# Performance work log

Hardware: AMD Instinct MI355X
Metric: run time of the kernel (lower is better)

Reference implementation:

```python
import jax, jax.numpy as jnp
import numpy as np
from jax import lax

# --- Clifford algebra Cl(3,0): sig_g = [1,1,1], n_blades = 8 ---
SIG = np.array([1.0, 1.0, 1.0], dtype=np.float32)
N_GEN = len(SIG)
N_BLADES = 1 << N_GEN

def _build_cayley(g):
    # Structure constants C[a,b,c]: e_a * e_b = C[a,b,a^b] * e_{a^b}
    n = len(g); nb = 1 << n
    C = np.zeros((nb, nb, nb), dtype=np.float32)
    for a in range(nb):
        for b in range(nb):
            s = 1.0
            x = a >> 1
            while x:
                if bin(x & b).count('1') % 2:
                    s = -s
                x >>= 1
            common = a & b
            for k in range(n):
                if (common >> k) & 1:
                    s *= g[k]
            C[a, b, a ^ b] = s
    return C

CAYLEY = _build_cayley(SIG)
# blade signs: scalar coefficient of e_i * e_i (metric square of each blade)
BLADE_SIGNS = np.array([CAYLEY[i, i, 0] for i in range(N_BLADES)], dtype=np.float32)

DT = 0.1      # EPEngine dt
N_FREE = 5    # EPEngine n_free

def _energy(h, input_mv, W_rec, C, signs):
    # h: [B,L,H,I]
    rho = jnp.clip(h, 0.0, 1.0)
    E_self = 0.5 * jnp.sum(h * h, axis=(1, 2, 3))                       # [B]
    E_in = jnp.einsum('blhi,blhi,i->b', rho, input_mv, signs)           # [B]
    # causal recurrent term: geometric product of h_{l-1} with W_rec
    rec = jnp.einsum('blhi,ghj,ijk->blgk', rho[:, :-1], W_rec, C)       # [B,L-1,H,I]
    E_rec = jnp.einsum('blhk,blhk,k->b', rho[:, 1:], rec, signs)        # [B]
    return E_self - E_in - E_rec

def _free_phase(h0, input_mv, W_rec, C, signs):
    gfn = jax.grad(lambda h: jnp.sum(_energy(h, input_mv, W_rec, C, signs)))
    def step(h, _):
        return h - DT * gfn(h), None
    h, _ = lax.scan(step, h0, None, length=N_FREE)
    return h

def setup_inputs() -> dict:
    key = jax.random.key(0)
    ks = jax.random.split(key, 5)
    B, L, V, E, H = 4, 256, 32000, 256, 256
    x = jax.random.randint(ks[0], (B, L), 0, V)
    emb_table = jax.random.normal(ks[1], (V, E), jnp.float32)
    W_in = jax.random.normal(ks[2], (H, E, N_BLADES), jnp.float32) * 0.1
    W_rec = jax.random.normal(ks[3], (H, H, N_BLADES), jnp.float32) * 0.05
    W_out = jax.random.normal(ks[4], (V, H, N_BLADES), jnp.float32) * 0.1
    return {"x": x, "emb_table": emb_table, "W_in": W_in, "W_rec": W_rec, "W_out": W_out}

def reference(x, emb_table, W_in, W_rec, W_out):
    C = jnp.asarray(CAYLEY)
    signs = jnp.asarray(BLADE_SIGNS)
    emb = emb_table[x]                                  # [B,L,E]
    input_mv = jnp.einsum('bld,hdi->blhi', emb, W_in)   # [B,L,H,I]
    B, L = x.shape
    H = W_in.shape[0]
    h0 = jnp.zeros((B, L, H, N_BLADES), jnp.float32)
    h_free = _free_phase(h0, input_mv, W_rec, C, signs) # [B,L,H,I]
    # scalar part of geometric product of h_free with W_out (only blade 0 kept)
    logits = jnp.einsum('blhi,vhj,ij->blv', h_free, W_out, C[:, :, 0])
    return logits
```

## Files before the change

### kernel.cpp

```cpp
#include <hip/hip_runtime.h>
#include <cstddef>
#include <cstdint>

#define VOCAB  32000
#define EMB    256
#define NB     8
#define KDIM   2048
#define NROWS  1024
#define NCOL   4096
#define LLEN   256

typedef __attribute__((ext_vector_type(8))) short short8;
typedef __attribute__((ext_vector_type(4))) float f32x4;
typedef __attribute__((ext_vector_type(16))) float f32x16;
typedef __attribute__((ext_vector_type(4))) int i32x4;
typedef __attribute__((ext_vector_type(16))) int i32x16;

__device__ __forceinline__ float cl3_sign(int a, int b) {
  int x = a >> 1, p = 0;
  while (x) { p ^= __popc(x & b) & 1; x >>= 1; }
  return p ? -1.f : 1.f;
}

__device__ __forceinline__ float clipf(float v) { return fminf(fmaxf(v, 0.f), 1.f); }

__device__ __forceinline__ unsigned short f2bf(float f) {
  unsigned u = __float_as_uint(f);
  u += 0x7FFF + ((u >> 16) & 1);
  return (unsigned short)(u >> 16);
}
__device__ __forceinline__ float bf2f(unsigned short h) {
  return __uint_as_float(((unsigned)h) << 16);
}

__device__ __forceinline__ void gload16(const void* g, void* l) {
  __builtin_amdgcn_global_load_lds((const __attribute__((address_space(1))) uint32_t*)g,
                                   (__attribute__((address_space(3))) uint32_t*)l, 16, 0, 0);
}

__device__ __forceinline__ float dig_inv(float mx) {
  return exp2f((float)(5 - ilogbf(fmaxf(mx, 1e-20f))));
}

__device__ __forceinline__ size_t bfoff(int rt, int k, int r) {
  return ((size_t)(rt * 128 + (k >> 4)) << 11) + (size_t)(((k >> 3) & 1) << 10) + ((r & 127) << 3) + (k & 7);
}

__global__ __launch_bounds__(256) void k_build_mrt(const float* __restrict__ Wrec,
                                                   unsigned short* __restrict__ Mhi,
                                                   unsigned short* __restrict__ Mlo) {
  const int t = threadIdx.x;
  const int b = blockIdx.x;
  if (b < 2048) {
    const int n = b, h = t;
    const int g = n >> 3, kb = n & 7;
    const float* src = Wrec + (size_t)g * KDIM + h * 8;
    float w[8];
    *(float4*)&w[0] = *(const float4*)src;
    *(float4*)&w[4] = *(const float4*)(src + 4);
    short8 H, L;
#pragma unroll
    for (int i = 0; i < 8; ++i) {
      int j = i ^ kb;
      float v = w[j] * cl3_sign(i, j);
      unsigned short hi = f2bf(v);
      H[i] = (short)hi;
      L[i] = (short)f2bf(v - bf2f(hi));
    }
    size_t off = ((size_t)((n >> 7) * 128 + (h >> 1)) << 11) + ((size_t)(h & 1) << 10) + ((n & 127) << 3);
    *(short8*)&Mhi[off] = H;
    *(short8*)&Mlo[off] = L;
  } else {
    const int h = b - 2048, p = t;
    const float* src = Wrec + (size_t)h * KDIM + p * 8;
    float w[8];
    *(float4*)&w[0] = *(const float4*)src;
    *(float4*)&w[4] = *(const float4*)(src + 4);
    const int slabn = 16 + (p >> 4);
    const size_t baseo = ((size_t)(slabn * 128 + (h >> 1)) << 11) + ((size_t)(h & 1) << 10);
#pragma unroll
    for (int q = 0; q < 8; ++q) {
      int r = (p & 15) * 8 + q;
      short8 H, L;
#pragma unroll
      for (int i = 0; i < 8; ++i) {
        int j = q ^ i;
        float v = cl3_sign(i, i) * cl3_sign(q, j) * w[j];
        unsigned short hi = f2bf(v);
        H[i] = (short)hi;
        L[i] = (short)f2bf(v - bf2f(hi));
      }
      size_t off = baseo + (r << 3);
      *(short8*)&Mhi[off] = H;
      *(short8*)&Mlo[off] = L;
    }
  }
}

__global__ __launch_bounds__(256) void k_dig_wout(const float* __restrict__ W,
                                                  float* __restrict__ sB,
                                                  char* __restrict__ Wd1,
                                                  char* __restrict__ Wd2) {
  __shared__ float ld[4 * 2052];
  __shared__ float rmax[4];
  const int t = threadIdx.x;
  const int bid = blockIdx.x;
  const float* src = W + (size_t)bid * 8192;
#pragma unroll
  for (int i = 0; i < 8; ++i) {
    int f = i * 256 + t;
    int row = f >> 9, c4 = f & 511;
    float4 v = ((const float4*)src)[f];
    *(float4*)&ld[row * 2052 + c4 * 4] = v;
  }
  __syncthreads();
  const int w = t >> 6, l = t & 63;
  float m = 0.f;
#pragma unroll
  for (int j = 0; j < 8; ++j) {
    float4 v = *(const float4*)&ld[w * 2052 + (j * 64 + l) * 4];
    m = fmaxf(m, fmaxf(fmaxf(fabsf(v.x), fabsf(v.y)), fmaxf(fabsf(v.z), fabsf(v.w))));
  }
#pragma unroll
  for (int s = 1; s < 64; s <<= 1) m = fmaxf(m, __shfl_xor(m, s));
  m = fmaxf(m, 1e-20f);
  if (l == 0) { rmax[w] = m; sB[bid * 4 + w] = exp2f((float)(ilogbf(m) + 2)); }
  __syncthreads();
  const int rloc = t & 3;
  const int rowg = bid * 4 + rloc;
  const int rowtile = rowg >> 7, rowin = rowg & 127;
  const float inv = dig_inv(rmax[rloc]);
#pragma unroll
  for (int it = 0; it < 2; ++it) {
    int c16 = (t >> 2) + it * 64;
    char d1[16], d2[16];
#pragma unroll
    for (int j = 0; j < 16; ++j) {
      float tv = ld[rloc * 2052 + c16 * 16 + j] * inv;
      float f1 = rintf(tv);
      d1[j] = (char)(int)f1;
      d2[j] = (char)(int)rintf((tv - f1) * 128.f);
    }
    size_t addr = ((size_t)(rowtile * 64 + (c16 >> 1)) << 12) + (size_t)((c16 & 1) << 11) + (rowin << 4);
    *(i32x4*)&Wd1[addr] = *(i32x4*)d1;
    *(i32x4*)&Wd2[addr] = *(i32x4*)d2;
  }
}

__global__ __launch_bounds__(256) void k_input_h1(const int* __restrict__ x,
                                                  const float* __restrict__ emb,
                                                  const float* __restrict__ Win,
                                                  float* __restrict__ Imv,
                                                  float* __restrict__ Hb,
                                                  unsigned short* __restrict__ Hhi,
                                                  unsigned short* __restrict__ Hlo) {
  __shared__ float se[4][EMB];
  int r0 = blockIdx.x * 4;
  int t = threadIdx.x;
  for (int rr = 0; rr < 4; ++rr) {
    int tok = x[r0 + rr];
    se[rr][t] = emb[(size_t)tok * EMB + t];
  }
  __syncthreads();
  float acc[4][8];
#pragma unroll
  for (int rr = 0; rr < 4; ++rr)
#pragma unroll
    for (int i = 0; i < 8; ++i) acc[rr][i] = 0.f;
  const float* wrow = Win + (size_t)t * KDIM;
  for (int d = 0; d < EMB; ++d) {
    float4 w0 = *(const float4*)(wrow + d * 8);
    float4 w1 = *(const float4*)(wrow + d * 8 + 4);
#pragma unroll
    for (int rr = 0; rr < 4; ++rr) {
      float e = se[rr][d];
      acc[rr][0] += e * w0.x; acc[rr][1] += e * w0.y;
      acc[rr][2] += e * w0.z; acc[rr][3] += e * w0.w;
      acc[rr][4] += e * w1.x; acc[rr][5] += e * w1.y;
      acc[rr][6] += e * w1.z; acc[rr][7] += e * w1.w;
    }
  }
  const int c = t * 8;
  for (int rr = 0; rr < 4; ++rr) {
    int r = r0 + rr;
    float* o = Imv + (size_t)r * KDIM + c;
    *(float4*)o = make_float4(acc[rr][0], acc[rr][1], acc[rr][2], acc[rr][3]);
    *(float4*)(o + 4) = make_float4(acc[rr][4], acc[rr][5], acc[rr][6], acc[rr][7]);
    float hn[8];
    short8 h8, l8;
#pragma unroll
    for (int j = 0; j < 8; ++j) {
      float f = acc[rr][j] * (((0xE8 >> j) & 1) ? -1.f : 1.f);
      hn[j] = 0.f - 0.1f * (0.f - 0.5f * f);
      float a = clipf(hn[j]);
      unsigned short hi = f2bf(a);
      h8[j] = (short)hi;
      l8[j] = (short)f2bf(a - bf2f(hi));
    }
    float* hb = Hb + (size_t)r * KDIM + c;
    *(float4*)hb = make_float4(hn[0], hn[1], hn[2], hn[3]);
    *(float4*)(hb + 4) = make_float4(hn[4], hn[5], hn[6], hn[7]);
    size_t off = bfoff(r >> 7, c, r);
    *(short8*)&Hhi[off] = h8;
    *(short8*)&Hlo[off] = l8;
  }
}

__global__ __launch_bounds__(256, 2) void k_gemm_pre(const unsigned short* __restrict__ Ahi,
                                                     const unsigned short* __restrict__ Alo,
                                                     const unsigned short* __restrict__ Bhi,
                                                     const unsigned short* __restrict__ Blo,
                                                     float* __restrict__ RF0,
                                                     float* __restrict__ RF1) {
  __shared__ __align__(16) char lds[3 * 16384];
  const int b = blockIdx.x;
  const int lin = (b & 7) * 64 + (b >> 3);
  const int half = lin >> 8;
  const int rest = lin & 255;
  const int tm = rest & 7, tn = rest >> 3;
  const int ktbase = half * 64;
  float* __restrict__ C = half ? RF1 : RF0;
  const int t = threadIdx.x;
  const int l = t & 63, w = t >> 6;
  const int wr = w >> 1, wc = w & 1;
  const int wo = w << 10;

  const char* aHg = (const char*)Ahi + (((size_t)(tm * 128 + ktbase)) << 12) + (t << 4);
  const char* aLg = (const char*)Alo + (((size_t)(tm * 128 + ktbase)) << 12) + (t << 4);
  const char* bHg = (const char*)Bhi + (((size_t)(tn * 128 + ktbase)) << 12) + (t << 4);
  const char* bLg = (const char*)Blo + (((size_t)(tn * 128 + ktbase)) << 12) + (t << 4);

  f32x16 acc[2][2];
#pragma unroll
  for (int i = 0; i < 2; ++i)
#pragma unroll
    for (int j = 0; j < 2; ++j) acc[i][j] = (f32x16)0.f;

  auto STAGE = [&](int bf, int kt) {
    char* lb = &lds[bf * 16384];
    size_t kb = (size_t)kt << 12;
    gload16(aHg + kb, lb + wo);
    gload16(aLg + kb, lb + 4096 + wo);
    gload16(bHg + kb, lb + 8192 + wo);
    gload16(bLg + kb, lb + 12288 + wo);
  };

  STAGE(0, 0); STAGE(1, 1);

  const int ra = wr * 64 + (l & 31);
  const int rb = wc * 64 + (l & 31);
  const int cho = (l >> 5) << 11;
  int cur = 0;
  for (int kt = 0; kt < 64; ++kt) {
    int pf = cur + 2; if (pf >= 3) pf -= 3;
    if (kt < 63) { asm volatile("s_waitcnt vmcnt(4)" ::: "memory"); }
    else         { asm volatile("s_waitcnt vmcnt(0)" ::: "memory"); }
    __builtin_amdgcn_s_barrier();
    const char* lb = &lds[cur * 16384];
    short8 ah[2], al[2], bh[2], bl[2];
#pragma unroll
    for (int mi = 0; mi < 2; ++mi) {
      int off = cho + ((ra + mi * 32) << 4);
      ah[mi] = *(const short8*)(lb + off);
      al[mi] = *(const short8*)(lb + 4096 + off);
    }
#pragma unroll
    for (int nj = 0; nj < 2; ++nj) {
      int off = cho + ((rb + nj * 32) << 4);
      bh[nj] = *(const short8*)(lb + 8192 + off);
      bl[nj] = *(const short8*)(lb + 12288 + off);
    }
    if (kt + 2 < 64) STAGE(pf, kt + 2);
    __builtin_amdgcn_s_setprio(1);
#pragma unroll
    for (int mi = 0; mi < 2; ++mi)
#pragma unroll
      for (int nj = 0; nj < 2; ++nj) {
        acc[mi][nj] = __builtin_amdgcn_mfma_f32_32x32x16_bf16(ah[mi], bh[nj], acc[mi][nj], 0, 0, 0);
        acc[mi][nj] = __builtin_amdgcn_mfma_f32_32x32x16_bf16(ah[mi], bl[nj], acc[mi][nj], 0, 0, 0);
        acc[mi][nj] = __builtin_amdgcn_mfma_f32_32x32x16_bf16(al[mi], bh[nj], acc[mi][nj], 0, 0, 0);
      }
    __builtin_amdgcn_s_setprio(0);
    cur = (cur == 2) ? 0 : cur + 1;
  }

  const int rg0 = tm * 128 + wr * 64 + ((l >> 5) << 2);
  const int cg0 = tn * 128 + wc * 64 + (l & 31);
#pragma unroll
  for (int mi = 0; mi < 2; ++mi)
#pragma unroll
    for (int nj = 0; nj < 2; ++nj) {
      f32x16 v = acc[mi][nj];
#pragma unroll
      for (int g = 0; g < 16; ++g) {
        int rr = (g & 3) + ((g >> 2) << 3);
        C[(size_t)(rg0 + mi * 32 + rr) * NCOL + cg0 + nj * 32] = v[g];
      }
    }
}

__global__ __launch_bounds__(256, 2) void k_gemm_i8(const char* __restrict__ Ad1,
                                                    const char* __restrict__ Ad2,
                                                    const char* __restrict__ Bd1,
                                                    const char* __restrict__ Bd2,
                                                    const float* __restrict__ sA,
                                                    const float* __restrict__ sB,
                                                    float* __restrict__ C) {
  __shared__ __align__(16) char lds[3 * 16384];
  const int b = blockIdx.x;
  const int lin = (b & 7) * 250 + (b >> 3);
  const int tm = lin & 7, tn = lin >> 3;
  const int t = threadIdx.x;
  const int l = t & 63, w = t >> 6;
  const int wr = w >> 1, wc = w & 1;
  const int wo = w << 10;

  const char* a1g = Ad1 + (((size_t)tm * 64) << 12) + (t << 4);
  const char* a2g = Ad2 + (((size_t)tm * 64) << 12) + (t << 4);
  const char* b1g = Bd1 + (((size_t)tn * 64) << 12) + (t << 4);
  const char* b2g = Bd2 + (((size_t)tn * 64) << 12) + (t << 4);

  i32x16 acc1[2][2], acc2[2][2];
#pragma unroll
  for (int i = 0; i < 2; ++i)
#pragma unroll
    for (int j = 0; j < 2; ++j) { acc1[i][j] = (i32x16)0; acc2[i][j] = (i32x16)0; }

  auto STAGE = [&](int bf, int kt) {
    char* lb = &lds[bf * 16384];
    size_t kb = (size_t)kt << 12;
    gload16(a1g + kb, lb + wo);
    gload16(a2g + kb, lb + 4096 + wo);
    gload16(b1g + kb, lb + 8192 + wo);
    gload16(b2g + kb, lb + 12288 + wo);
  };

  STAGE(0, 0); STAGE(1, 1);

  const int ra = wr * 64 + (l & 31);
  const int rb = wc * 64 + (l & 31);
  const int kqo = (l >> 5) << 11;
  int cur = 0;
  for (int kt = 0; kt < 64; ++kt) {
    int pf = cur + 2; if (pf >= 3) pf -= 3;
    if (kt < 63) { asm volatile("s_waitcnt vmcnt(4)" ::: "memory"); }
    else         { asm volatile("s_waitcnt vmcnt(0)" ::: "memory"); }
    __builtin_amdgcn_s_barrier();
    const char* lb = &lds[cur * 16384];
    i32x4 a1[2], a2[2], b1[2], b2[2];
#pragma unroll
    for (int mi = 0; mi < 2; ++mi) {
      int off = kqo + ((ra + mi * 32) << 4);
      a1[mi] = *(const i32x4*)(lb + off);
      a2[mi] = *(const i32x4*)(lb + 4096 + off);
    }
#pragma unroll
    for (int nj = 0; nj < 2; ++nj) {
      int off = kqo + ((rb + nj * 32) << 4);
      b1[nj] = *(const i32x4*)(lb + 8192 + off);
      b2[nj] = *(const i32x4*)(lb + 12288 + off);
    }
    if (kt + 2 < 64) STAGE(pf, kt + 2);
    __builtin_amdgcn_s_setprio(1);
#pragma unroll
    for (int mi = 0; mi < 2; ++mi)
#pragma unroll
      for (int nj = 0; nj < 2; ++nj) {
        acc1[mi][nj] = __builtin_amdgcn_mfma_i32_32x32x32_i8(a1[mi], b1[nj], acc1[mi][nj], 0, 0, 0);
        acc2[mi][nj] = __builtin_amdgcn_mfma_i32_32x32x32_i8(a1[mi], b2[nj], acc2[mi][nj], 0, 0, 0);
        acc2[mi][nj] = __builtin_amdgcn_mfma_i32_32x32x32_i8(a2[mi], b1[nj], acc2[mi][nj], 0, 0, 0);
      }
    __builtin_amdgcn_s_setprio(0);
    cur = (cur == 2) ? 0 : cur + 1;
  }

  const int rbase = tm * 128 + wr * 64 + ((l >> 5) << 2);
  const int cb = tn * 128 + wc * 64 + (l & 31);
#pragma unroll
  for (int mi = 0; mi < 2; ++mi)
#pragma unroll
    for (int nj = 0; nj < 2; ++nj) {
      float sBv = sB[cb + nj * 32] * (1.f / 16384.f);
#pragma unroll
      for (int g = 0; g < 16; ++g) {
        int rr = (g & 3) + ((g >> 2) << 3);
        int row = rbase + mi * 32 + rr;
        float c1 = sA[row] * sBv;
        C[(size_t)row * VOCAB + cb + nj * 32] =
            fmaf((float)acc2[mi][nj][g], c1 * (1.f / 128.f), (float)acc1[mi][nj][g] * c1);
      }
    }
}

template <int LAST>
__global__ __launch_bounds__(256) void k_update(float* __restrict__ Hb, const float* __restrict__ Imv,
                                                const float* __restrict__ RF0, const float* __restrict__ RF1,
                                                unsigned short* __restrict__ Hhi,
                                                unsigned short* __restrict__ Hlo,
                                                float* __restrict__ sA,
                                                char* __restrict__ Ad1,
                                                char* __restrict__ Ad2,
                                                int big) {
  __shared__ float red[256];
  int tix = threadIdx.x;
  int idx = blockIdx.x * 256 + tix;
  int r = idx >> 8;
  int c = (idx & 255) << 3;
  int m = r & (LLEN - 1);
  const size_t base = (size_t)r * KDIM + c;
  float h[8], f[8];
  *(float4*)&h[0] = *(const float4*)(Hb + base);
  *(float4*)&h[4] = *(const float4*)(Hb + base + 4);
  float4 i0 = *(const float4*)(Imv + base);
  float4 i1 = *(const float4*)(Imv + base + 4);
  f[0] = i0.x; f[1] = i0.y; f[2] = i0.z; f[3] = i0.w;
  f[4] = i1.x; f[5] = i1.y; f[6] = i1.z; f[7] = i1.w;
#pragma unroll
  for (int j = 0; j < 8; ++j) f[j] *= ((0xE8 >> j) & 1) ? -1.f : 1.f;
  if (m >= 1) {
    const float* rp0 = RF0 + (size_t)(r - 1) * NCOL + c;
    const float* rp1 = RF1 + (size_t)(r - 1) * NCOL + c;
#pragma unroll
    for (int j = 0; j < 8; ++j)
      f[j] += (rp0[j] + rp1[j]) * (((0xE8 >> j) & 1) ? -1.f : 1.f);
  }
  if (m < LLEN - 1) {
    const float* rn0 = RF0 + (size_t)(r + 1) * NCOL + KDIM + c;
    const float* rn1 = RF1 + (size_t)(r + 1) * NCOL + KDIM + c;
#pragma unroll
    for (int j = 0; j < 8; ++j) f[j] += rn0[j] + rn1[j];
  }
  float hn[8], av[8];
#pragma unroll
  for (int j = 0; j < 8; ++j) {
    float hv = h[j];
    float dr = (hv > 0.f && hv < 1.f) ? 1.f : ((hv == 0.f || hv == 1.f) ? 0.5f : 0.f);
    hn[j] = hv - 0.1f * (hv - dr * f[j]);
  }
  *(float4*)(Hb + base) = make_float4(hn[0], hn[1], hn[2], hn[3]);
  *(float4*)(Hb + base + 4) = make_float4(hn[4], hn[5], hn[6], hn[7]);
  if (!LAST) {
    short8 h8, l8;
#pragma unroll
    for (int j = 0; j < 8; ++j) {
      float a = clipf(hn[j]);
      unsigned short hi = f2bf(a);
      h8[j] = (short)hi;
      l8[j] = (short)f2bf(a - bf2f(hi));
    }
    size_t off = bfoff(r >> 7, c, r);
    *(short8*)&Hhi[off] = h8;
    *(short8*)&Hlo[off] = l8;
  } else {
    if (!big) return;
#pragma unroll
    for (int j = 0; j < 8; ++j) av[j] = hn[j] * (((0xE8 >> j) & 1) ? -1.f : 1.f);
    float lm = 0.f;
#pragma unroll
    for (int j = 0; j < 8; ++j) lm = fmaxf(lm, fabsf(av[j]));
    red[tix] = lm; __syncthreads();
    for (int s = 128; s; s >>= 1) { if (tix < s) red[tix] = fmaxf(red[tix], red[tix + s]); __syncthreads(); }
    float mx = fmaxf(red[0], 1e-20f);
    float inv = dig_inv(mx);
    if (tix == 0) sA[r] = exp2f((float)(ilogbf(mx) + 2));
    char d1[8], d2[8];
#pragma unroll
    for (int j = 0; j < 8; ++j) {
      float tv = av[j] * inv;
      float f1 = rintf(tv);
      d1[j] = (char)(int)f1;
      d2[j] = (char)(int)rintf((tv - f1) * 128.f);
    }
    size_t addr = ((size_t)((r >> 7) * 64 + (c >> 5)) << 12) + (size_t)(((c >> 4) & 1) << 11)
                + ((r & 127) << 4) + (c & 15);
    *(uint64_t*)&Ad1[addr] = *(uint64_t*)d1;
    *(uint64_t*)&Ad2[addr] = *(uint64_t*)d2;
  }
}

template <int AMODE>
__global__ __launch_bounds__(256) void k_gemm_split(const float* __restrict__ A,
                                                    const float* __restrict__ B,
                                                    float* __restrict__ C, int ldc) {
  __shared__ unsigned short Ah[128 * 32], Al[128 * 32];
  __shared__ unsigned short Bh[128 * 32], Bl[128 * 32];
  const int t = threadIdx.x;
  const int row0 = blockIdx.y * 128, col0 = blockIdx.x * 128;
  const int l = t & 63, w = t >> 6;
  const int wr = w >> 1, wc = w & 1;
  const int sr = t >> 3;
  const int cc = (t & 7) << 2;
  const int chunkb = cc >> 3;
  const int halfo = (cc >> 2) & 1;
  f32x4 acc[4][4];
#pragma unroll
  for (int i = 0; i < 4; ++i)
#pragma unroll
    for (int j = 0; j < 4; ++j) acc[i][j] = (f32x4)0.f;
  const float sA0 = 1.f;
  const float sA1 = (cc & 4) ? -1.f : 1.f;
  const float sA2 = sA1;
  const float sA3 = -1.f;
  for (int k0 = 0; k0 < KDIM; k0 += 32) {
    float4 va[4], vb[4];
#pragma unroll
    for (int i = 0; i < 4; ++i) {
      va[i] = *(const float4*)(A + (size_t)(row0 + sr + i * 32) * KDIM + k0 + cc);
      vb[i] = *(const float4*)(B + (size_t)(col0 + sr + i * 32) * KDIM + k0 + cc);
    }
    __syncthreads();
#pragma unroll
    for (int i = 0; i < 4; ++i) {
      int row = sr + i * 32;
      int idx = row * 32 + ((chunkb ^ (row & 3)) << 3) + (halfo << 2);
      float4 a = va[i];
      if (AMODE == 0) {
        a.x = clipf(a.x); a.y = clipf(a.y); a.z = clipf(a.z); a.w = clipf(a.w);
      } else {
        a.x *= sA0; a.y *= sA1; a.z *= sA2; a.w *= sA3;
      }
      ushort4 h4, l4;
      h4.x = f2bf(a.x); l4.x = f2bf(a.x - bf2f(h4.x));
      h4.y = f2bf(a.y); l4.y = f2bf(a.y - bf2f(h4.y));
      h4.z = f2bf(a.z); l4.z = f2bf(a.z - bf2f(h4.z));
      h4.w = f2bf(a.w); l4.w = f2bf(a.w - bf2f(h4.w));
      *(ushort4*)&Ah[idx] = h4;
      *(ushort4*)&Al[idx] = l4;
      float4 bb = vb[i];
      h4.x = f2bf(bb.x); l4.x = f2bf(bb.x - bf2f(h4.x));
      h4.y = f2bf(bb.y); l4.y = f2bf(bb.y - bf2f(h4.y));
      h4.z = f2bf(bb.z); l4.z = f2bf(bb.z - bf2f(h4.z));
      h4.w = f2bf(bb.w); l4.w = f2bf(bb.w - bf2f(h4.w));
      *(ushort4*)&Bh[idx] = h4;
      *(ushort4*)&Bl[idx] = l4;
    }
    __syncthreads();
    short8 ah[4], al[4], bh[4], bl[4];
#pragma unroll
    for (int mi = 0; mi < 4; ++mi) {
      int ar = wr * 64 + mi * 16 + (l & 15);
      int kc = (l >> 4) ^ (ar & 3);
      ah[mi] = *(short8*)&Ah[ar * 32 + kc * 8];
      al[mi] = *(short8*)&Al[ar * 32 + kc * 8];
      int br = wc * 64 + mi * 16 + (l & 15);
      int kb = (l >> 4) ^ (br & 3);
      bh[mi] = *(short8*)&Bh[br * 32 + kb * 8];
      bl[mi] = *(short8*)&Bl[br * 32 + kb * 8];
    }
#pragma unroll
    for (int mi = 0; mi < 4; ++mi)
#pragma unroll
      for (int ni = 0; ni < 4; ++ni) {
        acc[mi][ni] = __builtin_amdgcn_mfma_f32_16x16x32_bf16(ah[mi], bh[ni], acc[mi][ni], 0, 0, 0);
        acc[mi][ni] = __builtin_amdgcn_mfma_f32_16x16x32_bf16(ah[mi], bl[ni], acc[mi][ni], 0, 0, 0);
        acc[mi][ni] = __builtin_amdgcn_mfma_f32_16x16x32_bf16(al[mi], bh[ni], acc[mi][ni], 0, 0, 0);
      }
  }
#pragma unroll
  for (int mi = 0; mi < 4; ++mi)
#pragma unroll
    for (int ni = 0; ni < 4; ++ni) {
      int rg = row0 + wr * 64 + mi * 16 + (l >> 4) * 4;
      int cg = col0 + wc * 64 + ni * 16 + (l & 15);
#pragma unroll
      for (int j = 0; j < 4; ++j)
        C[(size_t)(rg + j) * ldc + cg] = acc[mi][ni][j];
    }
}

extern "C" void kernel_launch(void* const* d_in, const int* in_sizes, int n_in,
                              void* d_out, int out_size, void* d_ws, size_t ws_size,
                              hipStream_t stream) {
  const int*   x    = (const int*)d_in[0];
  const float* emb  = (const float*)d_in[1];
  const float* Win  = (const float*)d_in[2];
  const float* Wrec = (const float*)d_in[3];
  const float* Wout = (const float*)d_in[4];
  float* logits = (float*)d_out;

  char* base = (char*)d_ws;
  const size_t MB = 1ull << 20;
  float* Hbuf = (float*)(base + 0);
  float* Imv  = (float*)(base + 8 * MB);
  float* RF0  = (float*)(base + 16 * MB);
  float* RF1  = (float*)(base + 32 * MB);
  unsigned short* Hhi = (unsigned short*)(base + 48 * MB);
  unsigned short* Hlo = (unsigned short*)(base + 52 * MB);
  unsigned short* Mhi = (unsigned short*)(base + 56 * MB);
  unsigned short* Mlo = (unsigned short*)(base + 72 * MB);
  float* sA  = (float*)(base + 88 * MB);
  float* sB  = (float*)(base + 88 * MB + 4096);
  char* Wd1  = base + 88 * MB + 160 * 1024;
  char* Wd2  = Wd1 + (size_t)VOCAB * KDIM;
  char* Ad1  = (char*)Mhi;
  char* Ad2  = (char*)Mlo;

  const size_t need = (size_t)(Wd2 - base) + (size_t)VOCAB * KDIM;
  const bool big = ws_size >= need;

  k_build_mrt<<<2304, 256, 0, stream>>>(Wrec, Mhi, Mlo);
  k_input_h1<<<256, 256, 0, stream>>>(x, emb, Win, Imv, Hbuf, Hhi, Hlo);
  if (big) {
    k_dig_wout<<<8000, 256, 0, stream>>>(Wout, sB, Wd1, Wd2);
  }

  for (int it = 1; it < 5; ++it) {
    k_gemm_pre<<<512, 256, 0, stream>>>(Hhi, Hlo, Mhi, Mlo, RF0, RF1);
    if (it < 4) k_update<0><<<1024, 256, 0, stream>>>(Hbuf, Imv, RF0, RF1, Hhi, Hlo, sA, Ad1, Ad2, big);
    else        k_update<1><<<1024, 256, 0, stream>>>(Hbuf, Imv, RF0, RF1, Hhi, Hlo, sA, Ad1, Ad2, big);
  }

  if (big) {
    k_gemm_i8<<<2000, 256, 0, stream>>>(Ad1, Ad2, Wd1, Wd2, sA, sB, logits);
  } else {
    k_gemm_split<1><<<dim3(VOCAB / 128, NROWS / 128), 256, 0, stream>>>(Hbuf, Wout, logits, VOCAB);
  }
}
```

Baseline: 650.7 us.

## Load GEMM fragments directly from global memory instead of LDS staging

```diff
diff --git a/kernel.cpp b/kernel.cpp
--- a/kernel.cpp
+++ b/kernel.cpp
@@ -31,11 +31,6 @@
 }
 __device__ __forceinline__ float bf2f(unsigned short h) {
   return __uint_as_float(((unsigned)h) << 16);
-}
-
-__device__ __forceinline__ void gload16(const void* g, void* l) {
-  __builtin_amdgcn_global_load_lds((const __attribute__((address_space(1))) uint32_t*)g,
-                                   (__attribute__((address_space(3))) uint32_t*)l, 16, 0, 0);
 }
 
 __device__ __forceinline__ float dig_inv(float mx) {
@@ -212,7 +207,6 @@
                                                      const unsigned short* __restrict__ Blo,
                                                      float* __restrict__ RF0,
                                                      float* __restrict__ RF1) {
-  __shared__ __align__(16) char lds[3 * 16384];
   const int b = blockIdx.x;
   const int lin = (b & 7) * 64 + (b >> 3);
   const int half = lin >> 8;
@@ -223,54 +217,32 @@
   const int t = threadIdx.x;
   const int l = t & 63, w = t >> 6;
   const int wr = w >> 1, wc = w & 1;
-  const int wo = w << 10;
-
-  const char* aHg = (const char*)Ahi + (((size_t)(tm * 128 + ktbase)) << 12) + (t << 4);
-  const char* aLg = (const char*)Alo + (((size_t)(tm * 128 + ktbase)) << 12) + (t << 4);
-  const char* bHg = (const char*)Bhi + (((size_t)(tn * 128 + ktbase)) << 12) + (t << 4);
-  const char* bLg = (const char*)Blo + (((size_t)(tn * 128 + ktbase)) << 12) + (t << 4);
-
-  f32x16 acc[2][2];
-#pragma unroll
-  for (int i = 0; i < 2; ++i)
-#pragma unroll
-    for (int j = 0; j < 2; ++j) acc[i][j] = (f32x16)0.f;
-
-  auto STAGE = [&](int bf, int kt) {
-    char* lb = &lds[bf * 16384];
-    size_t kb = (size_t)kt << 12;
-    gload16(aHg + kb, lb + wo);
-    gload16(aLg + kb, lb + 4096 + wo);
-    gload16(bHg + kb, lb + 8192 + wo);
-    gload16(bLg + kb, lb + 12288 + wo);
-  };
-
-  STAGE(0, 0); STAGE(1, 1);
 
   const int ra = wr * 64 + (l & 31);
   const int rb = wc * 64 + (l & 31);
   const int cho = (l >> 5) << 11;
-  int cur = 0;
+
+  const size_t aOff = (((size_t)(tm * 128 + ktbase)) << 12) + cho + ((size_t)ra << 4);
+  const size_t bOff = (((size_t)(tn * 128 + ktbase)) << 12) + cho + ((size_t)rb << 4);
+  const char* aH = (const char*)Ahi + aOff;
+  const char* aL = (const char*)Alo + aOff;
+  const char* bH = (const char*)Bhi + bOff;
+  const char* bL = (const char*)Blo + bOff;
+
+  f32x16 acc[2][2];
+#pragma unroll
+  for (int i = 0; i < 2; ++i)
+#pragma unroll
+    for (int j = 0; j < 2; ++j) acc[i][j] = (f32x16)0.f;
+
+#pragma unroll 2
   for (int kt = 0; kt < 64; ++kt) {
-    int pf = cur + 2; if (pf >= 3) pf -= 3;
-    if (kt < 63) { asm volatile("s_waitcnt vmcnt(4)" ::: "memory"); }
-    else         { asm volatile("s_waitcnt vmcnt(0)" ::: "memory"); }
-    __builtin_amdgcn_s_barrier();
-    const char* lb = &lds[cur * 16384];
+    size_t o = (size_t)kt << 12;
     short8 ah[2], al[2], bh[2], bl[2];
-#pragma unroll
-    for (int mi = 0; mi < 2; ++mi) {
-      int off = cho + ((ra + mi * 32) << 4);
-      ah[mi] = *(const short8*)(lb + off);
-      al[mi] = *(const short8*)(lb + 4096 + off);
-    }
-#pragma unroll
-    for (int nj = 0; nj < 2; ++nj) {
-      int off = cho + ((rb + nj * 32) << 4);
-      bh[nj] = *(const short8*)(lb + 8192 + off);
-      bl[nj] = *(const short8*)(lb + 12288 + off);
-    }
-    if (kt + 2 < 64) STAGE(pf, kt + 2);
+    ah[0] = *(const short8*)(aH + o);        ah[1] = *(const short8*)(aH + o + 512);
+    al[0] = *(const short8*)(aL + o);        al[1] = *(const short8*)(aL + o + 512);
+    bh[0] = *(const short8*)(bH + o);        bh[1] = *(const short8*)(bH + o + 512);
+    bl[0] = *(const short8*)(bL + o);        bl[1] = *(const short8*)(bL + o + 512);
     __builtin_amdgcn_s_setprio(1);
 #pragma unroll
     for (int mi = 0; mi < 2; ++mi)
@@ -281,7 +253,6 @@
         acc[mi][nj] = __builtin_amdgcn_mfma_f32_32x32x16_bf16(al[mi], bh[nj], acc[mi][nj], 0, 0, 0);
       }
     __builtin_amdgcn_s_setprio(0);
-    cur = (cur == 2) ? 0 : cur + 1;
   }
 
   const int rg0 = tm * 128 + wr * 64 + ((l >> 5) << 2);
@@ -306,61 +277,38 @@
                                                     const float* __restrict__ sA,
                                                     const float* __restrict__ sB,
                                                     float* __restrict__ C) {
-  __shared__ __align__(16) char lds[3 * 16384];
   const int b = blockIdx.x;
   const int lin = (b & 7) * 250 + (b >> 3);
   const int tm = lin & 7, tn = lin >> 3;
   const int t = threadIdx.x;
   const int l = t & 63, w = t >> 6;
   const int wr = w >> 1, wc = w & 1;
-  const int wo = w << 10;
-
-  const char* a1g = Ad1 + (((size_t)tm * 64) << 12) + (t << 4);
-  const char* a2g = Ad2 + (((size_t)tm * 64) << 12) + (t << 4);
-  const char* b1g = Bd1 + (((size_t)tn * 64) << 12) + (t << 4);
-  const char* b2g = Bd2 + (((size_t)tn * 64) << 12) + (t << 4);
-
-  i32x16 acc1[2][2], acc2[2][2];
-#pragma unroll
-  for (int i = 0; i < 2; ++i)
-#pragma unroll
-    for (int j = 0; j < 2; ++j) { acc1[i][j] = (i32x16)0; acc2[i][j] = (i32x16)0; }
-
-  auto STAGE = [&](int bf, int kt) {
-    char* lb = &lds[bf * 16384];
-    size_t kb = (size_t)kt << 12;
-    gload16(a1g + kb, lb + wo);
-    gload16(a2g + kb, lb + 4096 + wo);
-    gload16(b1g + kb, lb + 8192 + wo);
-    gload16(b2g + kb, lb + 12288 + wo);
-  };
-
-  STAGE(0, 0); STAGE(1, 1);
 
   const int ra = wr * 64 + (l & 31);
   const int rb = wc * 64 + (l & 31);
   const int kqo = (l >> 5) << 11;
-  int cur = 0;
+
+  const size_t aOff = (((size_t)tm * 64) << 12) + kqo + ((size_t)ra << 4);
+  const size_t bOff = (((size_t)tn * 64) << 12) + kqo + ((size_t)rb << 4);
+  const char* a1p = Ad1 + aOff;
+  const char* a2p = Ad2 + aOff;
+  const char* b1p = Bd1 + bOff;
+  const char* b2p = Bd2 + bOff;
+
+  i32x16 acc1[2][2], acc2[2][2];
+#pragma unroll
+  for (int i = 0; i < 2; ++i)
+#pragma unroll
+    for (int j = 0; j < 2; ++j) { acc1[i][j] = (i32x16)0; acc2[i][j] = (i32x16)0; }
+
+#pragma unroll 2
   for (int kt = 0; kt < 64; ++kt) {
-    int pf = cur + 2; if (pf >= 3) pf -= 3;
-    if (kt < 63) { asm volatile("s_waitcnt vmcnt(4)" ::: "memory"); }
-    else         { asm volatile("s_waitcnt vmcnt(0)" ::: "memory"); }
-    __builtin_amdgcn_s_barrier();
-    const char* lb = &lds[cur * 16384];
+    size_t o = (size_t)kt << 12;
     i32x4 a1[2], a2[2], b1[2], b2[2];
-#pragma unroll
-    for (int mi = 0; mi < 2; ++mi) {
-      int off = kqo + ((ra + mi * 32) << 4);
-      a1[mi] = *(const i32x4*)(lb + off);
-      a2[mi] = *(const i32x4*)(lb + 4096 + off);
-    }
-#pragma unroll
-    for (int nj = 0; nj < 2; ++nj) {
-      int off = kqo + ((rb + nj * 32) << 4);
-      b1[nj] = *(const i32x4*)(lb + 8192 + off);
-      b2[nj] = *(const i32x4*)(lb + 12288 + off);
-    }
-    if (kt + 2 < 64) STAGE(pf, kt + 2);
+    a1[0] = *(const i32x4*)(a1p + o);        a1[1] = *(const i32x4*)(a1p + o + 512);
+    a2[0] = *(const i32x4*)(a2p + o);        a2[1] = *(const i32x4*)(a2p + o + 512);
+    b1[0] = *(const i32x4*)(b1p + o);        b1[1] = *(const i32x4*)(b1p + o + 512);
+    b2[0] = *(const i32x4*)(b2p + o);        b2[1] = *(const i32x4*)(b2p + o + 512);
     __builtin_amdgcn_s_setprio(1);
 #pragma unroll
     for (int mi = 0; mi < 2; ++mi)
@@ -371,7 +319,6 @@
         acc2[mi][nj] = __builtin_amdgcn_mfma_i32_32x32x32_i8(a2[mi], b1[nj], acc2[mi][nj], 0, 0, 0);
       }
     __builtin_amdgcn_s_setprio(0);
-    cur = (cur == 2) ? 0 : cur + 1;
   }
 
   const int rbase = tm * 128 + wr * 64 + ((l >> 5) << 2);
```

Result: slower. 766.3 us (+17.8%).
